# Optimization experiments

Hardware: AMD Instinct MI355X
Metric: run time of the kernel (lower is better)

The kernel has to match this reference:

```python
import jax, jax.numpy as jnp
import numpy as np
from jax import lax

V, D, N, K, E = 50000, 64, 32, 4, 2      # vocab, d_model, d_state, d_conv, expand
DI = E * D                                # d_inner = 128
R = max(1, D // 16)                       # dt_rank = 4
F = 4 * D                                 # ffn inner = 256
B, L = 1024, 200
EPS = 1e-12


def _ln(x, w, b):
    mu = jnp.mean(x, axis=-1, keepdims=True)
    var = jnp.mean((x - mu) ** 2, axis=-1, keepdims=True)
    return (x - mu) * lax.rsqrt(var + EPS) * w + b


def setup_inputs() -> dict:
    key = jax.random.key(0)
    ks = jax.random.split(key, 20)
    s = 0.02
    ids = jax.random.randint(ks[0], (B, L), 0, V)
    p = {
        'input_ids': ids,
        'emb': jax.random.normal(ks[1], (V, D), jnp.float32) * s,
        'ln_w': jnp.ones((D,), jnp.float32),
        'ln_b': jnp.zeros((D,), jnp.float32),
        'in_proj_w': jax.random.normal(ks[2], (2 * DI, D), jnp.float32) * s,
        'conv_w': jax.random.normal(ks[3], (DI, 1, K), jnp.float32) * 0.1,
        'conv_b': jnp.zeros((DI,), jnp.float32),
        'x_proj_w': jax.random.normal(ks[4], (R + 2 * N, DI), jnp.float32) * s,
        'dt_proj_w': jax.random.normal(ks[5], (DI, R), jnp.float32) * 0.1,
        'dt_proj_b': jax.random.normal(ks[6], (DI,), jnp.float32) * 0.1,
        'A_log': jnp.log(jnp.broadcast_to(jnp.arange(1, N + 1, dtype=jnp.float32), (DI, N))),
        'D_param': jnp.ones((DI,), jnp.float32),
        'out_proj_w': jax.random.normal(ks[7], (D, DI), jnp.float32) * s,
        'mln_w': jnp.ones((D,), jnp.float32),
        'mln_b': jnp.zeros((D,), jnp.float32),
        'ffn_w1': jax.random.normal(ks[8], (F, D), jnp.float32) * s,
        'ffn_b1': jnp.zeros((F,), jnp.float32),
        'ffn_w2': jax.random.normal(ks[9], (D, F), jnp.float32) * s,
        'ffn_b2': jnp.zeros((D,), jnp.float32),
        'fln_w': jnp.ones((D,), jnp.float32),
        'fln_b': jnp.zeros((D,), jnp.float32),
    }
    return p


def _forward(input_ids, emb, ln_w, ln_b, in_proj_w, conv_w, conv_b, x_proj_w,
             dt_proj_w, dt_proj_b, A_log, D_param, out_proj_w, mln_w, mln_b,
             ffn_w1, ffn_b1, ffn_w2, ffn_b2, fln_w, fln_b):
    # embedding (+dropout=identity in eval) + LayerNorm
    x = emb[input_ids]                            # [B,L,D]
    x = _ln(x, ln_w, ln_b)

    # --- Mamba block ---
    xz = jnp.einsum('bld,ed->ble', x, in_proj_w)  # [B,L,2*DI]
    xc, z = jnp.split(xz, 2, axis=-1)
    # depthwise causal conv over time
    xt = xc.transpose(0, 2, 1)                    # [B,DI,L]
    xt = lax.conv_general_dilated(xt, conv_w, (1,), [(K - 1, 0)],
                                  dimension_numbers=('NCH', 'OIH', 'NCH'),
                                  feature_group_count=DI)
    xt = xt + conv_b[None, :, None]
    xs = jax.nn.silu(xt.transpose(0, 2, 1))       # [B,L,DI]

    dbl = jnp.einsum('bld,ed->ble', xs, x_proj_w) # [B,L,R+2N]
    dt_lo, Bm, Cm = jnp.split(dbl, [R, R + N], axis=-1)
    dt = jax.nn.softplus(jnp.einsum('blr,dr->bld', dt_lo, dt_proj_w) + dt_proj_b)  # [B,L,DI]
    A = -jnp.exp(A_log)                           # [DI,N]

    def step(h, inp):
        dt_t, B_t, C_t, x_t = inp                 # [B,DI],[B,N],[B,N],[B,DI]
        dA = jnp.exp(dt_t[:, :, None] * A)        # [B,DI,N]
        h = dA * h + (dt_t * x_t)[:, :, None] * B_t[:, None, :]
        y = jnp.einsum('bdn,bn->bd', h, C_t)
        return h, y

    h0 = jnp.zeros((input_ids.shape[0], DI, N), dt.dtype)
    _, ys = lax.scan(step, h0, (dt.transpose(1, 0, 2), Bm.transpose(1, 0, 2),
                                Cm.transpose(1, 0, 2), xs.transpose(1, 0, 2)))
    y = ys.transpose(1, 0, 2) + D_param * xs      # [B,L,DI]
    y = y * jax.nn.silu(z)
    mout = jnp.einsum('ble,de->bld', y, out_proj_w)  # [B,L,D]

    # post-mamba LayerNorm (num_layers==1: no residual) + FFN
    hid = _ln(mout, mln_w, mln_b)
    f = jax.nn.gelu(jnp.einsum('bld,fd->blf', hid, ffn_w1) + ffn_b1)
    f = jnp.einsum('blf,df->bld', f, ffn_w2) + ffn_b2
    return _ln(f + hid, fln_w, fln_b)


def reference(input_ids, emb, ln_w, ln_b, in_proj_w, conv_w, conv_b, x_proj_w,
              dt_proj_w, dt_proj_b, A_log, D_param, out_proj_w, mln_w, mln_b,
              ffn_w1, ffn_b1, ffn_w2, ffn_b2, fln_w, fln_b):
    return _forward(input_ids, emb, ln_w, ln_b, in_proj_w, conv_w, conv_b,
                    x_proj_w, dt_proj_w, dt_proj_b, A_log, D_param, out_proj_w,
                    mln_w, mln_b, ffn_w1, ffn_b1, ffn_w2, ffn_b2, fln_w, fln_b)
```

## Files before the change

kernel.cpp:

```cpp
#include <hip/hip_runtime.h>
#include <hip/hip_bf16.h>

constexpr int Bn = 1024, Ln = 200, Dm = 64, DI = 128, Fh = 256;

#define DEVFN __device__ __forceinline__

typedef __attribute__((ext_vector_type(8))) short bf16x8;
typedef __attribute__((ext_vector_type(4))) float f32x4;

DEVFN float silu_(float x){ return x / (1.f + __expf(-x)); }
DEVFN float softplus_(float x){ return x > 20.f ? x : log1pf(__expf(x)); }
DEVFN float gelu_tanh_(float x){
  float c = 0.7978845608028654f * (x + 0.044715f * x * x * x);
  float e = __expf(2.f * c);
  float th = 1.f - 2.f / (e + 1.f);
  return 0.5f * x * (1.f + th);
}
DEVFN float wave64_sum(float v){
  #pragma unroll
  for (int off = 32; off; off >>= 1) v += __shfl_xor(v, off, 64);
  return v;
}
DEVFN unsigned short f2b(float f){
  unsigned int u = __float_as_uint(f);
  return (unsigned short)((u + 0x7fffu + ((u >> 16) & 1u)) >> 16);
}
DEVFN float b2f(unsigned short h){ return __uint_as_float(((unsigned int)h) << 16); }

__global__ __launch_bounds__(256)
void k1_embed_inproj(
    const int* __restrict__ ids, const float* __restrict__ emb,
    const float* __restrict__ lnw, const float* __restrict__ lnb,
    const float* __restrict__ ipw,
    unsigned short* __restrict__ xc, unsigned short* __restrict__ zy)
{
  __shared__ float xls[8][Dm];
  const int blk = blockIdx.x, b = blk / 5, t0 = (blk % 5) * 40;
  const int tid = threadIdx.x, wv = tid >> 6, ln = tid & 63;
  float wip[64];
  { const float4* p = (const float4*)(ipw + tid * Dm);
    #pragma unroll
    for (int k = 0; k < 16; k++) ((float4*)wip)[k] = p[k]; }
  const float lw = lnw[ln], lb = lnb[ln];
  const int* idb = ids + b * Ln;

  for (int sub = 0; sub < 5; sub++) {
    const int tt0 = t0 + sub * 8;
    #pragma unroll
    for (int s = 0; s < 2; s++) {
      int i = wv + 4 * s;
      float v = emb[(long)idb[tt0 + i] * Dm + ln];
      float mu  = wave64_sum(v) * (1.f / 64.f);
      float dv  = v - mu;
      float var = wave64_sum(dv * dv) * (1.f / 64.f);
      xls[i][ln] = dv * rsqrtf(var + 1e-12f) * lw + lb;
    }
    __syncthreads();
    #pragma unroll
    for (int i = 0; i < 8; i++) {
      const float4* xp = (const float4*)xls[i];
      float acc = 0.f;
      #pragma unroll
      for (int k = 0; k < 16; k++) {
        float4 x = xp[k];
        acc += wip[4*k+0]*x.x + wip[4*k+1]*x.y + wip[4*k+2]*x.z + wip[4*k+3]*x.w;
      }
      long idx = ((long)b * Ln + tt0 + i) * DI;
      unsigned short hv = f2b(acc);
      if (tid < DI) xc[idx + tid] = hv;
      else          zy[idx + tid - DI] = hv;
    }
    __syncthreads();
  }
}

__global__ __launch_bounds__(256)
void k2_conv_scan(
    const unsigned short* __restrict__ xc, unsigned short* __restrict__ zy,
    const float* __restrict__ cw, const float* __restrict__ cb,
    const float* __restrict__ xpw, const float* __restrict__ dtw, const float* __restrict__ dtb,
    const float* __restrict__ A_log, const float* __restrict__ Dp_g)
{
  constexpr int T = 8;
  __shared__ float xct[T + 3][DI];
  __shared__ float xs_s[T][132];
  __shared__ unsigned short z_s[T][DI];
  __shared__ unsigned short y_s[T][DI];
  __shared__ float psum[4][64 * 9];
  __shared__ float bc_s[T][68];
  __shared__ float dtlo_s[T][4];
  __shared__ float xpw_ext[4][DI];

  const int b = blockIdx.x, tid = threadIdx.x;
  const int wv = tid >> 6, ln = tid & 63;

  float wxp[32];
  { const float4* p = (const float4*)(xpw + ln * DI + wv * 32);
    #pragma unroll
    for (int k = 0; k < 8; k++) ((float4*)wxp)[k] = p[k]; }
  const int cd = tid & (DI - 1);
  const float4 cwv = *(const float4*)(cw + cd * 4);
  const float cbv = cb[cd];
  const int sd = tid >> 1, hf = tid & 1;
  const float4 dtwv = *(const float4*)(dtw + sd * 4);
  const float dtbv = dtb[sd], Dpv = Dp_g[sd];
  float A[16];
  { const float4* p = (const float4*)(A_log + sd * 32 + hf * 16);
    #pragma unroll
    for (int k = 0; k < 4; k++) {
      float4 v = p[k];
      A[4*k+0] = -__expf(v.x); A[4*k+1] = -__expf(v.y);
      A[4*k+2] = -__expf(v.z); A[4*k+3] = -__expf(v.w);
    } }
  float h[16];
  #pragma unroll
  for (int k = 0; k < 16; k++) h[k] = 0.f;

  for (int i = tid; i < 4 * DI; i += 256) xpw_ext[i >> 7][i & 127] = xpw[64 * DI + i];
  for (int i = tid; i < 3 * DI; i += 256) xct[i >> 7][i & 127] = 0.f;
  __syncthreads();

  for (int tile = 0; tile < 25; ++tile) {
    const int t0 = tile * T;
    const long gbase = ((long)b * Ln + t0) * DI;
    {
      ushort4 xv = ((const ushort4*)(xc + gbase))[tid];
      ushort4 zv = ((const ushort4*)(zy + gbase))[tid];
      int row = tid >> 5, col = (tid & 31) * 4;
      xct[3 + row][col + 0] = b2f(xv.x); xct[3 + row][col + 1] = b2f(xv.y);
      xct[3 + row][col + 2] = b2f(xv.z); xct[3 + row][col + 3] = b2f(xv.w);
      ((ushort4*)z_s)[tid] = zv;
    }
    __syncthreads();
    #pragma unroll
    for (int s = 0; s < 4; s++) {
      int tt = (tid >> 7) + 2 * s;
      float v = cbv + cwv.x * xct[tt + 0][cd] + cwv.y * xct[tt + 1][cd]
                    + cwv.z * xct[tt + 2][cd] + cwv.w * xct[tt + 3][cd];
      xs_s[tt][cd] = silu_(v);
    }
    __syncthreads();
    #pragma unroll
    for (int t = 0; t < T; t++) {
      const float4* xr = (const float4*)(&xs_s[t][wv * 32]);
      float a = 0.f;
      #pragma unroll
      for (int k = 0; k < 8; k++) {
        float4 x = xr[k];
        a += wxp[4*k+0]*x.x + wxp[4*k+1]*x.y + wxp[4*k+2]*x.z + wxp[4*k+3]*x.w;
      }
      psum[wv][ln * 9 + t] = a;
    }
    if (tid < 32) {
      int j = tid >> 3, t = tid & 7;
      const float4* wr = (const float4*)xpw_ext[j];
      const float4* xr = (const float4*)(&xs_s[t][0]);
      float a = 0.f;
      #pragma unroll
      for (int k = 0; k < 32; k++) {
        float4 w4 = wr[k]; float4 x = xr[k];
        a += w4.x*x.x + w4.y*x.y + w4.z*x.z + w4.w*x.w;
      }
      bc_s[t][60 + j] = a;
    }
    __syncthreads();
    #pragma unroll
    for (int s = 0; s < 2; s++) {
      int o = tid + 256 * s;
      int j = o >> 3, t = o & 7;
      float sum = psum[0][j*9+t] + psum[1][j*9+t] + psum[2][j*9+t] + psum[3][j*9+t];
      if (j < 4) dtlo_s[t][j] = sum;
      else       bc_s[t][j - 4] = sum;
    }
    __syncthreads();
    for (int t = 0; t < T; t++) {
      float4 dl = *(const float4*)dtlo_s[t];
      float dtv = softplus_(dtwv.x*dl.x + dtwv.y*dl.y + dtwv.z*dl.z + dtwv.w*dl.w + dtbv);
      float xsv = xs_s[t][sd];
      float zv  = b2f(z_s[t][sd]);
      float du  = dtv * xsv;
      const float4* bp = (const float4*)(&bc_s[t][hf * 16]);
      const float4* cp = (const float4*)(&bc_s[t][32 + hf * 16]);
      float y = 0.f;
      #pragma unroll
      for (int k = 0; k < 4; k++) {
        float4 Bv = bp[k], Cv = cp[k];
        float h0 = __expf(dtv*A[4*k+0]) * h[4*k+0] + du * Bv.x; h[4*k+0] = h0; y += h0 * Cv.x;
        float h1 = __expf(dtv*A[4*k+1]) * h[4*k+1] + du * Bv.y; h[4*k+1] = h1; y += h1 * Cv.y;
        float h2 = __expf(dtv*A[4*k+2]) * h[4*k+2] + du * Bv.z; h[4*k+2] = h2; y += h2 * Cv.z;
        float h3 = __expf(dtv*A[4*k+3]) * h[4*k+3] + du * Bv.w; h[4*k+3] = h3; y += h3 * Cv.w;
      }
      float yo = y + __shfl_xor(y, 1, 64);
      if (hf == 0)
        y_s[t][sd] = f2b((yo + Dpv * xsv) * silu_(zv));
    }
    __syncthreads();
    ((ushort4*)(zy + gbase))[tid] = ((ushort4*)y_s)[tid];
    for (int i = tid; i < 3 * DI; i += 256)
      xct[i >> 7][i & 127] = xct[8 + (i >> 7)][i & 127];
    __syncthreads();
  }
}

__global__ __launch_bounds__(256)
void k3a_op_ffn1(
    const unsigned short* __restrict__ y_g, const float* __restrict__ opw,
    const float* __restrict__ mlnw, const float* __restrict__ mlnb,
    const float* __restrict__ w1, const float* __restrict__ b1,
    unsigned short* __restrict__ hid_g, unsigned short* __restrict__ f_g)
{
  __shared__ unsigned short opwF[4][4][64][8];
  __shared__ unsigned short w1F[16][2][64][8];
  __shared__ unsigned short hidT[4][16][72];
  __shared__ float mlnw_s[64], mlnb_s[64], b1_s[Fh];
  const int tid = threadIdx.x, l = tid & 63, w = tid >> 6;

  for (int i = tid; i < 1024; i += 256) {
    int lane = i & 63, kc = (i >> 6) & 3, nt = i >> 8;
    const float* src = opw + (nt*16 + (lane & 15)) * DI + kc*32 + (lane >> 4)*8;
    unsigned short* dst = &opwF[nt][kc][lane][0];
    #pragma unroll
    for (int e = 0; e < 8; e++) dst[e] = f2b(src[e]);
  }
  for (int i = tid; i < 2048; i += 256) {
    int lane = i & 63, kc = (i >> 6) & 1, nt = i >> 7;
    const float* src = w1 + (nt*16 + (lane & 15)) * Dm + kc*32 + (lane >> 4)*8;
    unsigned short* dst = &w1F[nt][kc][lane][0];
    #pragma unroll
    for (int e = 0; e < 8; e++) dst[e] = f2b(src[e]);
  }
  if (tid < 64) { mlnw_s[tid] = mlnw[tid]; mlnb_s[tid] = mlnb[tid]; }
  b1_s[tid] = b1[tid];
  __syncthreads();

  const long tok0 = (long)blockIdx.x * 64 + w * 16;
  const int m = l & 15, kg = l >> 4;

  bf16x8 ya[4];
  { const unsigned short* yp = y_g + (tok0 + m) * DI + kg * 8;
    #pragma unroll
    for (int kc = 0; kc < 4; kc++) ya[kc] = *(const bf16x8*)(yp + kc * 32); }
  f32x4 acc[4];
  #pragma unroll
  for (int nt = 0; nt < 4; nt++) {
    f32x4 a = {0.f, 0.f, 0.f, 0.f};
    #pragma unroll
    for (int kc = 0; kc < 4; kc++)
      a = __builtin_amdgcn_mfma_f32_16x16x32_bf16(ya[kc], *(const bf16x8*)&opwF[nt][kc][l][0], a, 0, 0, 0);
    acc[nt] = a;
  }
  float mu[4], rs[4];
  #pragma unroll
  for (int r = 0; r < 4; r++) {
    float s = acc[0][r] + acc[1][r] + acc[2][r] + acc[3][r];
    #pragma unroll
    for (int off = 1; off < 16; off <<= 1) s += __shfl_xor(s, off, 64);
    mu[r] = s * (1.f / 64.f);
  }
  #pragma unroll
  for (int r = 0; r < 4; r++) {
    float q = 0.f;
    #pragma unroll
    for (int nt = 0; nt < 4; nt++) { float d = acc[nt][r] - mu[r]; q += d * d; }
    #pragma unroll
    for (int off = 1; off < 16; off <<= 1) q += __shfl_xor(q, off, 64);
    rs[r] = rsqrtf(q * (1.f / 64.f) + 1e-12f);
  }
  #pragma unroll
  for (int nt = 0; nt < 4; nt++) {
    int n = nt * 16 + (l & 15);
    float mwv = mlnw_s[n], mbv = mlnb_s[n];
    #pragma unroll
    for (int r = 0; r < 4; r++) {
      int mm = (l >> 4) * 4 + r;
      unsigned short hb = f2b((acc[nt][r] - mu[r]) * rs[r] * mwv + mbv);
      hidT[w][mm][n] = hb;
      hid_g[(tok0 + mm) * Dm + n] = hb;
    }
  }
  bf16x8 ha[2];
  #pragma unroll
  for (int kc = 0; kc < 2; kc++)
    ha[kc] = *(const bf16x8*)&hidT[w][m][kc * 32 + kg * 8];
  #pragma unroll
  for (int nt = 0; nt < 16; nt++) {
    f32x4 a = {0.f, 0.f, 0.f, 0.f};
    a = __builtin_amdgcn_mfma_f32_16x16x32_bf16(ha[0], *(const bf16x8*)&w1F[nt][0][l][0], a, 0, 0, 0);
    a = __builtin_amdgcn_mfma_f32_16x16x32_bf16(ha[1], *(const bf16x8*)&w1F[nt][1][l][0], a, 0, 0, 0);
    int n = nt * 16 + (l & 15);
    float bv = b1_s[n];
    #pragma unroll
    for (int r = 0; r < 4; r++) {
      int mm = (l >> 4) * 4 + r;
      f_g[(tok0 + mm) * Fh + n] = f2b(gelu_tanh_(a[r] + bv));
    }
  }
}

__global__ __launch_bounds__(256)
void k3b_ffn2(
    const unsigned short* __restrict__ f_g, const unsigned short* __restrict__ hid_g,
    const float* __restrict__ w2, const float* __restrict__ b2,
    const float* __restrict__ flnw, const float* __restrict__ flnb,
    float* __restrict__ out)
{
  __shared__ unsigned short w2F[4][8][64][8];
  __shared__ float b2_s[64], flw_s[64], flb_s[64];
  const int tid = threadIdx.x, l = tid & 63, w = tid >> 6;

  for (int i = tid; i < 2048; i += 256) {
    int lane = i & 63, kc = (i >> 6) & 7, nt = i >> 9;
    const float* src = w2 + (nt*16 + (lane & 15)) * Fh + kc*32 + (lane >> 4)*8;
    unsigned short* dst = &w2F[nt][kc][lane][0];
    #pragma unroll
    for (int e = 0; e < 8; e++) dst[e] = f2b(src[e]);
  }
  if (tid < 64) { b2_s[tid] = b2[tid]; flw_s[tid] = flnw[tid]; flb_s[tid] = flnb[tid]; }
  __syncthreads();

  const long tok0 = (long)blockIdx.x * 64 + w * 16;
  const int m = l & 15, kg = l >> 4;

  bf16x8 fa[8];
  { const unsigned short* fp = f_g + (tok0 + m) * Fh + kg * 8;
    #pragma unroll
    for (int kc = 0; kc < 8; kc++) fa[kc] = *(const bf16x8*)(fp + kc * 32); }
  f32x4 acc[4];
  #pragma unroll
  for (int nt = 0; nt < 4; nt++) {
    f32x4 a = {0.f, 0.f, 0.f, 0.f};
    #pragma unroll
    for (int kc = 0; kc < 8; kc++)
      a = __builtin_amdgcn_mfma_f32_16x16x32_bf16(fa[kc], *(const bf16x8*)&w2F[nt][kc][l][0], a, 0, 0, 0);
    acc[nt] = a;
  }
  #pragma unroll
  for (int nt = 0; nt < 4; nt++) {
    int n = nt * 16 + (l & 15);
    float bv = b2_s[n];
    #pragma unroll
    for (int r = 0; r < 4; r++) {
      int mm = (l >> 4) * 4 + r;
      acc[nt][r] += bv + b2f(hid_g[(tok0 + mm) * Dm + n]);
    }
  }
  float mu[4], rs[4];
  #pragma unroll
  for (int r = 0; r < 4; r++) {
    float s = acc[0][r] + acc[1][r] + acc[2][r] + acc[3][r];
    #pragma unroll
    for (int off = 1; off < 16; off <<= 1) s += __shfl_xor(s, off, 64);
    mu[r] = s * (1.f / 64.f);
  }
  #pragma unroll
  for (int r = 0; r < 4; r++) {
    float q = 0.f;
    #pragma unroll
    for (int nt = 0; nt < 4; nt++) { float d = acc[nt][r] - mu[r]; q += d * d; }
    #pragma unroll
    for (int off = 1; off < 16; off <<= 1) q += __shfl_xor(q, off, 64);
    rs[r] = rsqrtf(q * (1.f / 64.f) + 1e-12f);
  }
  #pragma unroll
  for (int nt = 0; nt < 4; nt++) {
    int n = nt * 16 + (l & 15);
    float fwv = flw_s[n], fbv = flb_s[n];
    #pragma unroll
    for (int r = 0; r < 4; r++) {
      int mm = (l >> 4) * 4 + r;
      out[(tok0 + mm) * Dm + n] = (acc[nt][r] - mu[r]) * rs[r] * fwv + fbv;
    }
  }
}

extern "C" void kernel_launch(void* const* d_in, const int* in_sizes, int n_in,
                              void* d_out, int out_size, void* d_ws, size_t ws_size,
                              hipStream_t stream)
{
  const int*   ids  = (const int*)  d_in[0];
  const float* emb  = (const float*)d_in[1];
  const float* lnw  = (const float*)d_in[2];
  const float* lnb  = (const float*)d_in[3];
  const float* ipw  = (const float*)d_in[4];
  const float* cw   = (const float*)d_in[5];
  const float* cb   = (const float*)d_in[6];
  const float* xpw  = (const float*)d_in[7];
  const float* dtw  = (const float*)d_in[8];
  const float* dtb  = (const float*)d_in[9];
  const float* alog = (const float*)d_in[10];
  const float* Dp   = (const float*)d_in[11];
  const float* opw  = (const float*)d_in[12];
  const float* mlnw = (const float*)d_in[13];
  const float* mlnb = (const float*)d_in[14];
  const float* w1   = (const float*)d_in[15];
  const float* b1   = (const float*)d_in[16];
  const float* w2   = (const float*)d_in[17];
  const float* b2   = (const float*)d_in[18];
  const float* flnw = (const float*)d_in[19];
  const float* flnb = (const float*)d_in[20];
  float* out = (float*)d_out;

  const size_t half = (size_t)Bn * Ln * DI * sizeof(unsigned short);
  char* ws = (char*)d_ws;
  unsigned short* xc   = (unsigned short*)ws;
  unsigned short* zy   = (unsigned short*)(ws + half);
  unsigned short* hid  = (unsigned short*)ws;
  unsigned short* fact = (unsigned short*)(ws + 2 * half);

  k1_embed_inproj<<<Bn * 5, 256, 0, stream>>>(ids, emb, lnw, lnb, ipw, xc, zy);
  k2_conv_scan<<<Bn, 256, 0, stream>>>(xc, zy, cw, cb, xpw, dtw, dtb, alog, Dp);
  k3a_op_ffn1<<<(Bn * Ln) / 64, 256, 0, stream>>>(zy, opw, mlnw, mlnb, w1, b1, hid, fact);
  k3b_ffn2<<<(Bn * Ln) / 64, 256, 0, stream>>>(fact, hid, w2, b2, flnw, flnb, out);
}
```

Baseline: 909.1 us.

## Split conv and x_proj into a parallel MFMA kernel ahead of the scan

The causal conv, SiLU and x_proj GEMM move out of the per-batch sequential scan kernel into a separate kernel tiled over 64-token blocks. That kernel computes x_proj with bf16 MFMA and writes xs, dt-low-rank and B/C to workspace. The scan kernel then only loads precomputed values per tile, which cuts its per-step syncs and FMA work. In exchange there is extra global traffic for the intermediates, bf16 rounding of B/C and xs, and one more launch.

```diff
diff --git a/kernel.cpp b/kernel.cpp
--- a/kernel.cpp
+++ b/kernel.cpp
@@ -75,32 +75,105 @@
 }
 
 __global__ __launch_bounds__(256)
-void k2_conv_scan(
-    const unsigned short* __restrict__ xc, unsigned short* __restrict__ zy,
+void k2a_conv_xproj(
+    const unsigned short* __restrict__ xc,
     const float* __restrict__ cw, const float* __restrict__ cb,
-    const float* __restrict__ xpw, const float* __restrict__ dtw, const float* __restrict__ dtb,
+    const float* __restrict__ xpw,
+    unsigned short* __restrict__ xs_g, float* __restrict__ dtlo_g,
+    unsigned short* __restrict__ bc_g)
+{
+  __shared__ unsigned short xctS[67 * 128];
+  __shared__ unsigned short xsS[64 * 144];
+  __shared__ unsigned short xpwF[5][4][64][8];
+  const int tid = threadIdx.x, l = tid & 63, w = tid >> 6;
+  const long tok0 = (long)blockIdx.x * 64;
+
+  for (int i = tid; i < 1280; i += 256) {
+    int lane = i & 63, kc = (i >> 6) & 3, nt = i >> 8;
+    int row = nt * 16 + (lane & 15);
+    unsigned short* dst = &xpwF[nt][kc][lane][0];
+    if (row < 68) {
+      const float* src = xpw + row * DI + kc * 32 + (lane >> 4) * 8;
+      #pragma unroll
+      for (int e = 0; e < 8; e++) dst[e] = f2b(src[e]);
+    } else {
+      #pragma unroll
+      for (int e = 0; e < 8; e++) dst[e] = 0;
+    }
+  }
+  for (int i = tid; i < 67 * 32; i += 256) {
+    int rr = i >> 5, c4 = i & 31;
+    long ft = tok0 - 3 + rr;
+    ushort4 v;
+    if (ft >= 0) v = ((const ushort4*)(xc + ft * DI))[c4];
+    else { v.x = 0; v.y = 0; v.z = 0; v.w = 0; }
+    ((ushort4*)xctS)[rr * 32 + c4] = v;
+  }
+  __syncthreads();
+
+  {
+    const int d4 = (tid & 31) * 4;
+    const int base200 = (int)(tok0 % 200);
+    float4 cv[4]; float cbr[4];
+    #pragma unroll
+    for (int c = 0; c < 4; c++) { cv[c] = *(const float4*)(cw + (d4 + c) * 4); cbr[c] = cb[d4 + c]; }
+    for (int t = tid >> 5; t < 64; t += 8) {
+      int p = base200 + t; if (p >= 200) p -= 200;
+      ushort4 r0 = *(const ushort4*)&xctS[(t + 0) * 128 + d4];
+      ushort4 r1 = *(const ushort4*)&xctS[(t + 1) * 128 + d4];
+      ushort4 r2 = *(const ushort4*)&xctS[(t + 2) * 128 + d4];
+      ushort4 r3 = *(const ushort4*)&xctS[(t + 3) * 128 + d4];
+      float m0 = (p >= 3) ? 1.f : 0.f, m1 = (p >= 2) ? 1.f : 0.f, m2 = (p >= 1) ? 1.f : 0.f;
+      ushort4 o;
+      { float a = cbr[0] + m0*cv[0].x*b2f(r0.x) + m1*cv[0].y*b2f(r1.x) + m2*cv[0].z*b2f(r2.x) + cv[0].w*b2f(r3.x); o.x = f2b(silu_(a)); }
+      { float a = cbr[1] + m0*cv[1].x*b2f(r0.y) + m1*cv[1].y*b2f(r1.y) + m2*cv[1].z*b2f(r2.y) + cv[1].w*b2f(r3.y); o.y = f2b(silu_(a)); }
+      { float a = cbr[2] + m0*cv[2].x*b2f(r0.z) + m1*cv[2].y*b2f(r1.z) + m2*cv[2].z*b2f(r2.z) + cv[2].w*b2f(r3.z); o.z = f2b(silu_(a)); }
+      { float a = cbr[3] + m0*cv[3].x*b2f(r0.w) + m1*cv[3].y*b2f(r1.w) + m2*cv[3].z*b2f(r2.w) + cv[3].w*b2f(r3.w); o.w = f2b(silu_(a)); }
+      *(ushort4*)&xsS[t * 144 + d4] = o;
+      *(ushort4*)(xs_g + (tok0 + t) * DI + d4) = o;
+    }
+  }
+  __syncthreads();
+
+  {
+    const int m = l & 15, kg = l >> 4;
+    const int tr = w * 16 + m;
+    bf16x8 xa[4];
+    #pragma unroll
+    for (int kc = 0; kc < 4; kc++)
+      xa[kc] = *(const bf16x8*)&xsS[tr * 144 + kc * 32 + kg * 8];
+    #pragma unroll
+    for (int nt = 0; nt < 5; nt++) {
+      f32x4 a = {0.f, 0.f, 0.f, 0.f};
+      #pragma unroll
+      for (int kc = 0; kc < 4; kc++)
+        a = __builtin_amdgcn_mfma_f32_16x16x32_bf16(xa[kc], *(const bf16x8*)&xpwF[nt][kc][l][0], a, 0, 0, 0);
+      int j = nt * 16 + m;
+      #pragma unroll
+      for (int r = 0; r < 4; r++) {
+        long mm = tok0 + w * 16 + (l >> 4) * 4 + r;
+        if (j < 4)       dtlo_g[mm * 4 + j] = a[r];
+        else if (j < 68) bc_g[mm * 64 + (j - 4)] = f2b(a[r]);
+      }
+    }
+  }
+}
+
+__global__ __launch_bounds__(256)
+void k2b_scan(
+    const unsigned short* __restrict__ xs_g, unsigned short* __restrict__ zy,
+    const unsigned short* __restrict__ bc_g, const float* __restrict__ dtlo_g,
+    const float* __restrict__ dtw, const float* __restrict__ dtb,
     const float* __restrict__ A_log, const float* __restrict__ Dp_g)
 {
   constexpr int T = 8;
-  __shared__ float xct[T + 3][DI];
-  __shared__ float xs_s[T][132];
+  __shared__ unsigned short xs_s[T][DI];
   __shared__ unsigned short z_s[T][DI];
   __shared__ unsigned short y_s[T][DI];
-  __shared__ float psum[4][64 * 9];
   __shared__ float bc_s[T][68];
-  __shared__ float dtlo_s[T][4];
-  __shared__ float xpw_ext[4][DI];
+  __shared__ float dtlo_s[Ln][4];
 
   const int b = blockIdx.x, tid = threadIdx.x;
-  const int wv = tid >> 6, ln = tid & 63;
-
-  float wxp[32];
-  { const float4* p = (const float4*)(xpw + ln * DI + wv * 32);
-    #pragma unroll
-    for (int k = 0; k < 8; k++) ((float4*)wxp)[k] = p[k]; }
-  const int cd = tid & (DI - 1);
-  const float4 cwv = *(const float4*)(cw + cd * 4);
-  const float cbv = cb[cd];
   const int sd = tid >> 1, hf = tid & 1;
   const float4 dtwv = *(const float4*)(dtw + sd * 4);
   const float dtbv = dtb[sd], Dpv = Dp_g[sd];
@@ -116,67 +189,26 @@
   #pragma unroll
   for (int k = 0; k < 16; k++) h[k] = 0.f;
 
-  for (int i = tid; i < 4 * DI; i += 256) xpw_ext[i >> 7][i & 127] = xpw[64 * DI + i];
-  for (int i = tid; i < 3 * DI; i += 256) xct[i >> 7][i & 127] = 0.f;
-  __syncthreads();
+  { const float4* src = (const float4*)(dtlo_g + (long)b * Ln * 4);
+    float4* dst = (float4*)dtlo_s;
+    for (int i = tid; i < Ln; i += 256) dst[i] = src[i]; }
 
   for (int tile = 0; tile < 25; ++tile) {
     const int t0 = tile * T;
     const long gbase = ((long)b * Ln + t0) * DI;
-    {
-      ushort4 xv = ((const ushort4*)(xc + gbase))[tid];
-      ushort4 zv = ((const ushort4*)(zy + gbase))[tid];
-      int row = tid >> 5, col = (tid & 31) * 4;
-      xct[3 + row][col + 0] = b2f(xv.x); xct[3 + row][col + 1] = b2f(xv.y);
-      xct[3 + row][col + 2] = b2f(xv.z); xct[3 + row][col + 3] = b2f(xv.w);
-      ((ushort4*)z_s)[tid] = zv;
-    }
-    __syncthreads();
-    #pragma unroll
-    for (int s = 0; s < 4; s++) {
-      int tt = (tid >> 7) + 2 * s;
-      float v = cbv + cwv.x * xct[tt + 0][cd] + cwv.y * xct[tt + 1][cd]
-                    + cwv.z * xct[tt + 2][cd] + cwv.w * xct[tt + 3][cd];
-      xs_s[tt][cd] = silu_(v);
-    }
-    __syncthreads();
-    #pragma unroll
-    for (int t = 0; t < T; t++) {
-      const float4* xr = (const float4*)(&xs_s[t][wv * 32]);
-      float a = 0.f;
-      #pragma unroll
-      for (int k = 0; k < 8; k++) {
-        float4 x = xr[k];
-        a += wxp[4*k+0]*x.x + wxp[4*k+1]*x.y + wxp[4*k+2]*x.z + wxp[4*k+3]*x.w;
-      }
-      psum[wv][ln * 9 + t] = a;
-    }
-    if (tid < 32) {
-      int j = tid >> 3, t = tid & 7;
-      const float4* wr = (const float4*)xpw_ext[j];
-      const float4* xr = (const float4*)(&xs_s[t][0]);
-      float a = 0.f;
-      #pragma unroll
-      for (int k = 0; k < 32; k++) {
-        float4 w4 = wr[k]; float4 x = xr[k];
-        a += w4.x*x.x + w4.y*x.y + w4.z*x.z + w4.w*x.w;
-      }
-      bc_s[t][60 + j] = a;
-    }
-    __syncthreads();
-    #pragma unroll
-    for (int s = 0; s < 2; s++) {
-      int o = tid + 256 * s;
-      int j = o >> 3, t = o & 7;
-      float sum = psum[0][j*9+t] + psum[1][j*9+t] + psum[2][j*9+t] + psum[3][j*9+t];
-      if (j < 4) dtlo_s[t][j] = sum;
-      else       bc_s[t][j - 4] = sum;
+    ((ushort4*)xs_s)[tid] = ((const ushort4*)(xs_g + gbase))[tid];
+    ((ushort4*)z_s)[tid]  = ((const ushort4*)(zy + gbase))[tid];
+    if (tid < 128) {
+      int t = tid >> 4, c4 = (tid & 15) * 4;
+      ushort4 v = ((const ushort4*)(bc_g + ((long)b * Ln + t0) * 64))[tid];
+      bc_s[t][c4 + 0] = b2f(v.x); bc_s[t][c4 + 1] = b2f(v.y);
+      bc_s[t][c4 + 2] = b2f(v.z); bc_s[t][c4 + 3] = b2f(v.w);
     }
     __syncthreads();
     for (int t = 0; t < T; t++) {
-      float4 dl = *(const float4*)dtlo_s[t];
+      float4 dl = *(const float4*)dtlo_s[t0 + t];
       float dtv = softplus_(dtwv.x*dl.x + dtwv.y*dl.y + dtwv.z*dl.z + dtwv.w*dl.w + dtbv);
-      float xsv = xs_s[t][sd];
+      float xsv = b2f(xs_s[t][sd]);
       float zv  = b2f(z_s[t][sd]);
       float du  = dtv * xsv;
       const float4* bp = (const float4*)(&bc_s[t][hf * 16]);
@@ -196,9 +228,6 @@
     }
     __syncthreads();
     ((ushort4*)(zy + gbase))[tid] = ((ushort4*)y_s)[tid];
-    for (int i = tid; i < 3 * DI; i += 256)
-      xct[i >> 7][i & 127] = xct[8 + (i >> 7)][i & 127];
-    __syncthreads();
   }
 }
 
@@ -401,14 +430,19 @@
   float* out = (float*)d_out;
 
   const size_t half = (size_t)Bn * Ln * DI * sizeof(unsigned short);
+  const long M = (long)Bn * Ln;
   char* ws = (char*)d_ws;
   unsigned short* xc   = (unsigned short*)ws;
   unsigned short* zy   = (unsigned short*)(ws + half);
+  unsigned short* xs   = (unsigned short*)(ws + 2 * half);
+  unsigned short* bc   = (unsigned short*)(ws + 3 * half);
+  float*          dtlo = (float*)(ws + 3 * half + M * 64 * 2);
   unsigned short* hid  = (unsigned short*)ws;
   unsigned short* fact = (unsigned short*)(ws + 2 * half);
 
   k1_embed_inproj<<<Bn * 5, 256, 0, stream>>>(ids, emb, lnw, lnb, ipw, xc, zy);
-  k2_conv_scan<<<Bn, 256, 0, stream>>>(xc, zy, cw, cb, xpw, dtw, dtb, alog, Dp);
-  k3a_op_ffn1<<<(Bn * Ln) / 64, 256, 0, stream>>>(zy, opw, mlnw, mlnb, w1, b1, hid, fact);
-  k3b_ffn2<<<(Bn * Ln) / 64, 256, 0, stream>>>(fact, hid, w2, b2, flnw, flnb, out);
-}
+  k2a_conv_xproj<<<(int)(M / 64), 256, 0, stream>>>(xc, cw, cb, xpw, xs, dtlo, bc);
+  k2b_scan<<<Bn, 256, 0, stream>>>(xs, zy, bc, dtlo, dtw, dtb, alog, Dp);
+  k3a_op_ffn1<<<(int)(M / 64), 256, 0, stream>>>(zy, opw, mlnw, mlnb, w1, b1, hid, fact);
+  k3b_ffn2<<<(int)(M / 64), 256, 0, stream>>>(fact, hid, w2, b2, flnw, flnb, out);
+}
```

After: 791.6 us. -12.9%, faster.
